# Kernel optimization log

Hardware: AMD Instinct MI355X
Metric: run time of the kernel (lower is better)

The kernel has to match this reference:

```python
import jax, jax.numpy as jnp
import numpy as np
from jax import lax

B, C, N = 128, 320, 256
H = W = 16
GROUPS = 5
RATIO = 8
MASK_EPS = 1e-6   # registered buffer 'eps' in the torch module
GN_EPS = 1e-5     # torch GroupNorm default


def setup_inputs() -> dict:
    key = jax.random.key(0)
    ks = jax.random.split(key, 10)
    def rn(k, shape, scale=0.05):
        return jax.random.normal(k, shape, dtype=jnp.float32) * scale
    return {
        "x": jax.random.normal(ks[0], (B, C, N), dtype=jnp.float32),
        "low_cutoff": jnp.float32(0.2),
        "high_cutoff": jnp.float32(0.7),
        "ca_w1": rn(ks[1], (C // RATIO, C)),
        "ca_b1": jnp.zeros((C // RATIO,), jnp.float32),
        "ca_w2": rn(ks[2], (3 * C, C // RATIO)),
        "ca_b2": jnp.zeros((3 * C,), jnp.float32),
        "low_w": rn(ks[3], (C, C, 3, 3)),
        "low_b": jnp.zeros((C,), jnp.float32),
        "low_g": jnp.ones((C,), jnp.float32),
        "low_beta": jnp.zeros((C,), jnp.float32),
        "mid_w": rn(ks[4], (C, C, 3, 3)),
        "mid_b": jnp.zeros((C,), jnp.float32),
        "mid_g": jnp.ones((C,), jnp.float32),
        "mid_beta": jnp.zeros((C,), jnp.float32),
        "high_w": rn(ks[5], (C, C, 3, 3)),
        "high_b": jnp.zeros((C,), jnp.float32),
        "high_g": jnp.ones((C,), jnp.float32),
        "high_beta": jnp.zeros((C,), jnp.float32),
        "sa_w": rn(ks[6], (1, C, 1, 1)),
        "sa_b": jnp.zeros((1,), jnp.float32),
    }


def _conv3x3_gn(y, w, b, gamma, beta):
    # Conv2d(C,C,3,padding=1) -> GroupNorm(5,C)
    out = lax.conv_general_dilated(
        y, w, window_strides=(1, 1), padding='SAME',
        dimension_numbers=('NCHW', 'OIHW', 'NCHW'))
    out = out + b[None, :, None, None]
    b_, c_, h_, w_ = out.shape
    g = out.reshape(b_, GROUPS, c_ // GROUPS, h_, w_)
    mu = g.mean(axis=(2, 3, 4), keepdims=True)
    var = g.var(axis=(2, 3, 4), keepdims=True)
    g = (g - mu) * lax.rsqrt(var + GN_EPS)
    out = g.reshape(b_, c_, h_, w_)
    return out * gamma[None, :, None, None] + beta[None, :, None, None]


def reference(x, low_cutoff, high_cutoff, ca_w1, ca_b1, ca_w2, ca_b2,
              low_w, low_b, low_g, low_beta,
              mid_w, mid_b, mid_g, mid_beta,
              high_w, high_b, high_g, high_beta,
              sa_w, sa_b):
    b, c, n = x.shape
    n_pix = H * W
    # reshape_to_square (N == n_pix here, pad/slice kept for faithfulness)
    if n < n_pix:
        xp = jnp.pad(x, ((0, 0), (0, 0), (0, n_pix - n)))
    else:
        xp = x[:, :, :n_pix]
    x2d = xp.reshape(b, c, H, W)

    # DynamicFrequencyFilter: avgpool over N -> 1x1 conv1d -> relu -> 1x1 conv1d -> sigmoid
    avg = x.mean(axis=-1)                                  # [B, C]
    hcw = jax.nn.relu(avg @ ca_w1.T + ca_b1)               # [B, C//8]
    cw = jax.nn.sigmoid(hcw @ ca_w2.T + ca_b2)             # [B, 3C]
    cw = cw.reshape(b, 3, c, 1, 1)

    # FFT + shifted frequency masks. torch fftshift(dim=None) shifts all dims,
    # but the B/C shifts commute with the (B/C-broadcast) mask multiply and are
    # undone by ifftshift, so shifting only the spatial axes is equivalent.
    fft_feat = jnp.fft.fftshift(jnp.fft.fft2(x2d), axes=(-2, -1))
    yy, xx = jnp.meshgrid(jnp.linspace(-1.0, 1.0, H), jnp.linspace(-1.0, 1.0, W), indexing='ij')
    dist = jnp.sqrt(xx ** 2 + yy ** 2) / np.sqrt(2.0)
    low_mask = jax.nn.sigmoid((low_cutoff - dist) / MASK_EPS)
    mid_mask = jax.nn.sigmoid((dist - low_cutoff) / MASK_EPS) * jax.nn.sigmoid((high_cutoff - dist) / MASK_EPS)
    high_mask = jax.nn.sigmoid((dist - high_cutoff) / MASK_EPS)

    def band(mask):
        return jnp.fft.ifft2(jnp.fft.ifftshift(fft_feat * mask, axes=(-2, -1))).real

    low_feat = _conv3x3_gn(band(low_mask), low_w, low_b, low_g, low_beta) + x2d
    mid_feat = _conv3x3_gn(band(mid_mask), mid_w, mid_b, mid_g, mid_beta) + x2d
    high_feat = _conv3x3_gn(band(high_mask), high_w, high_b, high_g, high_beta) + x2d

    fused = cw[:, 0] * low_feat + cw[:, 1] * mid_feat + cw[:, 2] * high_feat

    # spatial attention: 1x1 conv C->1, sigmoid
    sw = jax.nn.sigmoid(jnp.einsum('bchw,c->bhw', fused, sa_w[0, :, 0, 0])[:, None] + sa_b[0])
    out = (fused * sw).reshape(b, c, n_pix)
    return out[:, :, :n]
```

## Files before the change

### kernel.cpp

```cpp
#include <hip/hip_runtime.h>
#include <math.h>

#define NB 128
#define NC 320
#define NG 5
#define CPG 64
#define NHID 40

typedef short bf16x8 __attribute__((ext_vector_type(8)));
typedef short s16x4  __attribute__((ext_vector_type(4)));
typedef float f32x4  __attribute__((ext_vector_type(4)));

__device__ __forceinline__ float sigf(float x){ return 1.0f/(1.0f+expf(-x)); }

__device__ __forceinline__ unsigned short f2b(float f){
  unsigned u = __float_as_uint(f);
  unsigned r = (u + 0x7fffu + ((u >> 16) & 1u)) >> 16;
  return (unsigned short)r;
}
__device__ __forceinline__ float b2f(unsigned short u){
  return __uint_as_float(((unsigned)u) << 16);
}

__device__ __forceinline__ void gll16(const void* g, void* l){
  __builtin_amdgcn_global_load_lds(
      (const __attribute__((address_space(1))) void*)g,
      (__attribute__((address_space(3))) void*)l, 16, 0, 0);
}

__global__ __launch_bounds__(256) void k_mask(const float* __restrict__ lowc,
                                              const float* __restrict__ highc,
                                              float* __restrict__ mask){
  int t = threadIdx.x;
  int a1 = t >> 4, a2 = t & 15;
  float lc = lowc[0], hc = highc[0];
  const float step = 2.0f / 15.0f;
  float cy = -1.0f + step * (float)a1;
  float cx = -1.0f + step * (float)a2;
  float dist = sqrtf(cx*cx + cy*cy) / 1.41421356237309515f;
  mask[t]       = sigf((lc - dist) * 1e6f);
  mask[256 + t] = sigf((dist - lc) * 1e6f) * sigf((hc - dist) * 1e6f);
  mask[512 + t] = sigf((dist - hc) * 1e6f);
}

__global__ __launch_bounds__(256) void k_prepWgT(const float* __restrict__ mask,
                                                 unsigned short* __restrict__ WgT){
  __shared__ float cost[16];
  __shared__ float msh[256];
  int band = blockIdx.x >> 8, p = blockIdx.x & 255;
  int q = threadIdx.x;
  if (q < 16) cost[q] = cosf((float)q * 0.392699081698724154f);
  msh[q] = mask[band*256 + q];
  __syncthreads();
  int d1 = ((p >> 4) - (q >> 4)) & 15;
  int d2 = ((p & 15) - (q & 15)) & 15;
  float s = 0.f;
  int ang0 = (8*d1 + 8*d2) & 15;
  for (int a1 = 0; a1 < 16; ++a1){
    int ang = (ang0 + a1*d1) & 15;
    #pragma unroll
    for (int a2 = 0; a2 < 16; ++a2){
      s += msh[a1*16 + a2] * cost[ang];
      ang = (ang + d2) & 15;
    }
  }
  WgT[(size_t)(band << 16) + (p << 8) + q] = f2b(s * (1.0f/256.0f));
}

__global__ __launch_bounds__(320) void k_wt2(const float* __restrict__ w0,
                                             const float* __restrict__ w1,
                                             const float* __restrict__ w2,
                                             unsigned short* __restrict__ WAb){
  int band = blockIdx.x / 360, blk = blockIdx.x % 360;
  const float* w = band == 0 ? w0 : (band == 1 ? w1 : w2);
  int co  = threadIdx.x;
  int tap = blk / 40; int rem = blk % 40; int cib = rem >> 2; int cig = rem & 3;
  unsigned short tmp[8];
  #pragma unroll
  for (int j = 0; j < 8; ++j){
    int ci = cib*32 + cig*8 + j;
    tmp[j] = f2b(w[((size_t)co * NC + ci) * 9 + tap]);
  }
  unsigned short* dst = WAb + (size_t)band*921600 + ((size_t)blk * NC + co) * 8;
  *(s16x4*)dst       = *(s16x4*)tmp;
  *(s16x4*)(dst + 4) = *(s16x4*)(tmp + 4);
}

__global__ __launch_bounds__(256) void k_zerohalo(unsigned short* __restrict__ bandT){
  unsigned short* base = bandT + (size_t)blockIdx.x * 103680;
  for (int i = threadIdx.x; i < 5440; i += 256){
    int idx = i / 80, v = i % 80;
    int r, c;
    if (idx < 18)      { r = 0;        c = idx;      }
    else if (idx < 36) { r = 17;       c = idx - 18; }
    else if (idx < 52) { r = idx - 35; c = 0;        }
    else               { r = idx - 51; c = 17;       }
    s16x4 z = {0,0,0,0};
    *(s16x4*)(base + (size_t)(r*18 + c)*NC + v*4) = z;
  }
}

__global__ __launch_bounds__(256) void k_ca(const float* __restrict__ avg,
                                            const float* __restrict__ w1,
                                            const float* __restrict__ b1,
                                            const float* __restrict__ w2,
                                            const float* __restrict__ b2,
                                            float* __restrict__ cw){
  __shared__ float a[NC];
  __shared__ float h[NHID];
  int b = blockIdx.x, t = threadIdx.x;
  a[t] = avg[b * NC + t];
  if (t < NC - 256) a[256 + t] = avg[b * NC + 256 + t];
  __syncthreads();
  if (t < NHID){
    float s = b1[t];
    for (int i = 0; i < NC; ++i) s += w1[t * NC + i] * a[i];
    h[t] = fmaxf(s, 0.0f);
  }
  __syncthreads();
  for (int o = t; o < 3 * NC; o += 256){
    float s = b2[o];
    for (int i = 0; i < NHID; ++i) s += w2[o * NHID + i] * h[i];
    cw[b * (3 * NC) + o] = sigf(s);
  }
}

__global__ __launch_bounds__(256, 4) void k_bandg3(const float* __restrict__ x,
                                                   const unsigned short* __restrict__ WgT,
                                                   unsigned short* __restrict__ bandT,
                                                   float* __restrict__ avgOut){
  __shared__ unsigned short xt[64*256];
  int tid = threadIdx.x;
  int wgid = (blockIdx.x & 7)*80 + (blockIdx.x >> 3);
  int b = wgid / 5, cq = wgid % 5;
  int cibase = cq * 64;
  size_t rowbase = (size_t)wgid * 64;

  {
    int r = tid >> 2, c0 = (tid & 3) * 64;
    const float* xp = x + (rowbase + r)*256 + c0;
    unsigned short* dp = xt + r*256;
    int sw = (r & 7) << 3;
    float rs = 0.f;
    #pragma unroll
    for (int j = 0; j < 64; j += 4){
      float4 f = *(const float4*)(xp + j);
      rs += f.x + f.y + f.z + f.w;
      unsigned short t4[4] = { f2b(f.x), f2b(f.y), f2b(f.z), f2b(f.w) };
      *(s16x4*)(dp + ((c0 + j) ^ sw)) = *(s16x4*)t4;
    }
    rs += __shfl_down(rs, 1);
    rs += __shfl_down(rs, 2);
    if ((tid & 3) == 0) avgOut[rowbase + r] = rs * (1.0f/256.0f);
  }
  __syncthreads();

  int l  = tid & 63;
  int wq = tid >> 6;
  int cig = l >> 4, lan = l & 15;

  for (int band = 0; band < 3; ++band){
    const unsigned short* Wg = WgT + (size_t)band * 65536;
    unsigned short* bT = bandT + (size_t)band * 13271040;

    f32x4 acc[4][4];
    #pragma unroll
    for (int m = 0; m < 4; ++m)
      #pragma unroll
      for (int n = 0; n < 4; ++n) acc[m][n] = (f32x4){0.f,0.f,0.f,0.f};

    #pragma unroll 2
    for (int ks = 0; ks < 8; ++ks){
      int koff = ks*32 + cig*8;
      bf16x8 a[4], bv[4];
      #pragma unroll
      for (int m = 0; m < 4; ++m){
        int row = m*16 + lan;
        a[m] = *(const bf16x8*)(xt + row*256 + (koff ^ ((row & 7) << 3)));
      }
      #pragma unroll
      for (int n = 0; n < 4; ++n){
        int p = wq*64 + n*16 + lan;
        bv[n] = *(const bf16x8*)(Wg + (size_t)p*256 + koff);
      }
      #pragma unroll
      for (int m = 0; m < 4; ++m)
        #pragma unroll
        for (int n = 0; n < 4; ++n)
          acc[m][n] = __builtin_amdgcn_mfma_f32_16x16x32_bf16(a[m], bv[n], acc[m][n], 0, 0, 0);
    }

    #pragma unroll
    for (int m = 0; m < 4; ++m){
      #pragma unroll
      for (int n = 0; n < 4; ++n){
        int p = wq*64 + n*16 + lan;
        int slot = ((p >> 4) + 1) * 18 + (p & 15) + 1;
        int ci = cibase + m*16 + cig*4;
        unsigned short o[4] = { f2b(acc[m][n][0]), f2b(acc[m][n][1]),
                                f2b(acc[m][n][2]), f2b(acc[m][n][3]) };
        *(s16x4*)(bT + ((size_t)(b*324 + slot))*NC + ci) = *(s16x4*)o;
      }
    }
  }
}

__global__ __launch_bounds__(256, 3) void k_convg(const unsigned short* __restrict__ bandT,
                                                  const unsigned short* __restrict__ WAb,
                                                  const float* __restrict__ bias0,
                                                  const float* __restrict__ bias1,
                                                  const float* __restrict__ bias2,
                                                  unsigned short* __restrict__ convb,
                                                  float* __restrict__ stats_part){
  __shared__ char ldsA[2*10240];
  __shared__ char ldsB[2*11520];
  __shared__ float stw[4][5][2];

  int tid = threadIdx.x;
  int wgid = (blockIdx.x & 7)*192 + (blockIdx.x >> 3);
  int band = wgid / 512; int rem = wgid & 511;
  int b = rem >> 2, ch = (rem >> 1) & 1, ph = rem & 1;

  const unsigned short* bT = bandT + (size_t)band*13271040 + (size_t)b*103680;
  const unsigned short* WA = WAb + (size_t)band*921600;
  const float* bias = band == 0 ? bias0 : (band == 1 ? bias1 : bias2);
  unsigned short* cb = convb + (size_t)band * 10485760;

  int l = tid & 63, w = tid >> 6;
  int wco = w >> 1, wpx = w & 1;
  int cig = l >> 4, lan = l & 15;
  int cobase = ch*160 + wco*80;
  int px0 = ph*128 + wpx*64;

  int ga0 = tid, ga1 = tid + 256, ga2 = tid + 512;
  int aoff0 = (ga0/160)*2560 + (ga0%160)*8 + ch*1280;
  int aoff1 = (ga1/160)*2560 + (ga1%160)*8 + ch*1280;
  int aoff2 = (ga2/160)*2560 + (ga2%160)*8 + ch*1280;
  int gb0 = tid, gb1 = tid + 256, gb2 = tid + 512;
  int boff0 = (ph*144 + gb0%180)*320 + (gb0/180)*8;
  int boff1 = (ph*144 + gb1%180)*320 + (gb1/180)*8;
  int boff2 = (ph*144 + gb2%180)*320 + (gb2/180)*8;

  int Aread0 = (cig*160 + wco*80 + lan)*16;
  int Bread0 = (cig*180 + (wpx*4 + 1)*18 + lan + 1)*16;

  f32x4 acc[5][4];
  #pragma unroll
  for (int m = 0; m < 5; ++m)
    #pragma unroll
    for (int n = 0; n < 4; ++n) acc[m][n] = (f32x4){0.f,0.f,0.f,0.f};

#define STAGE_A(KN) do { \
    int tap_ = (KN)%9, cib_ = (KN)/9; \
    const unsigned short* sA = WA + (size_t)(tap_*40 + cib_*4)*2560; \
    char* dA = ldsA + ((KN)&1)*10240; \
    gll16(sA + aoff0, dA + tid*16); \
    gll16(sA + aoff1, dA + 4096 + tid*16); \
    if (tid < 128) gll16(sA + aoff2, dA + 8192 + tid*16); \
  } while(0)

#define STAGE_B(CN) do { \
    const unsigned short* sB = bT + (CN)*32; \
    char* dB = ldsB + ((CN)&1)*11520; \
    gll16(sB + boff0, dB + tid*16); \
    gll16(sB + boff1, dB + 4096 + tid*16); \
    if (tid < 208) gll16(sB + boff2, dB + 8192 + tid*16); \
  } while(0)

  STAGE_A(0);
  STAGE_B(0);
  __syncthreads();

  for (int kk = 0; kk < 90; ++kk){
    int cib = kk / 9;
    int tap = kk - cib*9;

    if (kk < 89) STAGE_A(kk + 1);
    if (tap == 0 && cib < 9) STAGE_B(cib + 1);

    int dhdw = ((tap/3)*18 + (tap - (tap/3)*3) - 19)*16;

    const char* Ab = ldsA + (kk&1)*10240 + Aread0;
    bf16x8 a0 = *(const bf16x8*)(Ab);
    bf16x8 a1 = *(const bf16x8*)(Ab + 256);
    bf16x8 a2 = *(const bf16x8*)(Ab + 512);
    bf16x8 a3 = *(const bf16x8*)(Ab + 768);
    bf16x8 a4 = *(const bf16x8*)(Ab + 1024);
    const char* Bb = ldsB + (cib&1)*11520 + Bread0 + dhdw;
    bf16x8 b0 = *(const bf16x8*)(Bb);
    bf16x8 b1 = *(const bf16x8*)(Bb + 288);
    bf16x8 b2 = *(const bf16x8*)(Bb + 576);
    bf16x8 b3 = *(const bf16x8*)(Bb + 864);

    __builtin_amdgcn_s_setprio(1);
    acc[0][0] = __builtin_amdgcn_mfma_f32_16x16x32_bf16(a0, b0, acc[0][0],0,0,0);
    acc[0][1] = __builtin_amdgcn_mfma_f32_16x16x32_bf16(a0, b1, acc[0][1],0,0,0);
    acc[0][2] = __builtin_amdgcn_mfma_f32_16x16x32_bf16(a0, b2, acc[0][2],0,0,0);
    acc[0][3] = __builtin_amdgcn_mfma_f32_16x16x32_bf16(a0, b3, acc[0][3],0,0,0);
    acc[1][0] = __builtin_amdgcn_mfma_f32_16x16x32_bf16(a1, b0, acc[1][0],0,0,0);
    acc[1][1] = __builtin_amdgcn_mfma_f32_16x16x32_bf16(a1, b1, acc[1][1],0,0,0);
    acc[1][2] = __builtin_amdgcn_mfma_f32_16x16x32_bf16(a1, b2, acc[1][2],0,0,0);
    acc[1][3] = __builtin_amdgcn_mfma_f32_16x16x32_bf16(a1, b3, acc[1][3],0,0,0);
    acc[2][0] = __builtin_amdgcn_mfma_f32_16x16x32_bf16(a2, b0, acc[2][0],0,0,0);
    acc[2][1] = __builtin_amdgcn_mfma_f32_16x16x32_bf16(a2, b1, acc[2][1],0,0,0);
    acc[2][2] = __builtin_amdgcn_mfma_f32_16x16x32_bf16(a2, b2, acc[2][2],0,0,0);
    acc[2][3] = __builtin_amdgcn_mfma_f32_16x16x32_bf16(a2, b3, acc[2][3],0,0,0);
    acc[3][0] = __builtin_amdgcn_mfma_f32_16x16x32_bf16(a3, b0, acc[3][0],0,0,0);
    acc[3][1] = __builtin_amdgcn_mfma_f32_16x16x32_bf16(a3, b1, acc[3][1],0,0,0);
    acc[3][2] = __builtin_amdgcn_mfma_f32_16x16x32_bf16(a3, b2, acc[3][2],0,0,0);
    acc[3][3] = __builtin_amdgcn_mfma_f32_16x16x32_bf16(a3, b3, acc[3][3],0,0,0);
    acc[4][0] = __builtin_amdgcn_mfma_f32_16x16x32_bf16(a4, b0, acc[4][0],0,0,0);
    acc[4][1] = __builtin_amdgcn_mfma_f32_16x16x32_bf16(a4, b1, acc[4][1],0,0,0);
    acc[4][2] = __builtin_amdgcn_mfma_f32_16x16x32_bf16(a4, b2, acc[4][2],0,0,0);
    acc[4][3] = __builtin_amdgcn_mfma_f32_16x16x32_bf16(a4, b3, acc[4][3],0,0,0);
    __builtin_amdgcn_s_setprio(0);

    __syncthreads();
  }
#undef STAGE_A
#undef STAGE_B

  #pragma unroll
  for (int m = 0; m < 5; ++m)
    #pragma unroll
    for (int r = 0; r < 4; ++r){
      float bvs = bias[cobase + m*16 + cig*4 + r];
      #pragma unroll
      for (int n = 0; n < 4; ++n) acc[m][n][r] += bvs;
    }

  #pragma unroll
  for (int m = 0; m < 5; ++m){
    float s = 0.f, q = 0.f;
    #pragma unroll
    for (int n = 0; n < 4; ++n)
      #pragma unroll
      for (int r = 0; r < 4; ++r){ float v = acc[m][n][r]; s += v; q += v*v; }
    #pragma unroll
    for (int o = 32; o > 0; o >>= 1){ s += __shfl_xor(s, o); q += __shfl_xor(q, o); }
    if (l == 0){ stw[w][m][0] = s; stw[w][m][1] = q; }
  }

  #pragma unroll
  for (int m = 0; m < 5; ++m)
    #pragma unroll
    for (int r = 0; r < 4; ++r){
      int co = cobase + m*16 + cig*4 + r;
      unsigned short* op = cb + ((size_t)(b*NC + co))*256 + px0 + lan;
      #pragma unroll
      for (int n = 0; n < 4; ++n) op[n*16] = f2b(acc[m][n][r]);
    }

  __syncthreads();
  if (tid < 6){
    int gl = tid >> 1, comp = tid & 1;
    int g = ch*2 + gl;
    float t = 0.f;
    for (int w2 = 0; w2 < 4; ++w2)
      #pragma unroll
      for (int m = 0; m < 5; ++m)
        if (((ch*160 + (w2 >> 1)*80 + m*16) >> 6) == g) t += stw[w2][m][comp];
    stats_part[((size_t)(band*NB + b)*NG + g)*8 + ch*4 + ph*2 + comp] = t;
  }
}

__global__ __launch_bounds__(512) void k_fuse3(const unsigned short* __restrict__ cb0,
                                               const unsigned short* __restrict__ cb1,
                                               const unsigned short* __restrict__ cb2,
                                               const float* __restrict__ x,
                                               const float* __restrict__ stats_part,
                                               const float* __restrict__ g0, const float* __restrict__ be0,
                                               const float* __restrict__ g1, const float* __restrict__ be1,
                                               const float* __restrict__ g2, const float* __restrict__ be2,
                                               const float* __restrict__ cw,
                                               const float* __restrict__ saw,
                                               const float* __restrict__ sab,
                                               float* __restrict__ out){
  __shared__ unsigned short fl[NC*128];
  __shared__ float mu_s[3][NG], rs_s[3][NG], sh[4][128];
  int b = blockIdx.x >> 1, half = blockIdx.x & 1;
  int tid = threadIdx.x;
  if (tid < 15){
    int band = tid / 5, g = tid % 5;
    const float* sp = stats_part + ((size_t)(band*NB + b)*NG + g)*8;
    float s = 0.f, q = 0.f;
    if (g <= 2){ s += sp[0] + sp[2]; q += sp[1] + sp[3]; }
    if (g >= 2){ s += sp[4] + sp[6]; q += sp[5] + sp[7]; }
    float mu = s * (1.f/16384.f);
    float var = q * (1.f/16384.f) - mu*mu;
    mu_s[band][g] = mu; rs_s[band][g] = rsqrtf(var + 1e-5f);
  }
  __syncthreads();

  int p = tid & 127, cs = tid >> 7;
  int px = half*128 + p;
  float sacc = 0.f;
  const float* cwb = cw + b*960;
  for (int ci = cs; ci < NC; ci += 4){
    int g = ci >> 6;
    size_t idx = ((size_t)(b*NC + ci))*256 + px;
    float xv = x[idx];
    float f =
      cwb[ci      ] * ((b2f(cb0[idx]) - mu_s[0][g])*rs_s[0][g]*g0[ci] + be0[ci] + xv) +
      cwb[320 + ci] * ((b2f(cb1[idx]) - mu_s[1][g])*rs_s[1][g]*g1[ci] + be1[ci] + xv) +
      cwb[640 + ci] * ((b2f(cb2[idx]) - mu_s[2][g])*rs_s[2][g]*g2[ci] + be2[ci] + xv);
    fl[ci*128 + p] = f2b(f);
    sacc += f * saw[ci];
  }
  sh[cs][p] = sacc;
  __syncthreads();
  if (tid < 128) sh[0][tid] = sigf(sh[0][tid] + sh[1][tid] + sh[2][tid] + sh[3][tid] + sab[0]);
  __syncthreads();
  float swv = sh[0][p];
  for (int ci = cs; ci < NC; ci += 4){
    size_t idx = ((size_t)(b*NC + ci))*256 + px;
    out[idx] = b2f(fl[ci*128 + p]) * swv;
  }
}

extern "C" void kernel_launch(void* const* d_in, const int* in_sizes, int n_in,
                              void* d_out, int out_size, void* d_ws, size_t ws_size,
                              hipStream_t stream){
  (void)in_sizes; (void)n_in; (void)out_size; (void)ws_size;
  const float* x     = (const float*)d_in[0];
  const float* lowc  = (const float*)d_in[1];
  const float* highc = (const float*)d_in[2];
  const float* ca_w1 = (const float*)d_in[3];
  const float* ca_b1 = (const float*)d_in[4];
  const float* ca_w2 = (const float*)d_in[5];
  const float* ca_b2 = (const float*)d_in[6];
  const float* conv_w[3] = {(const float*)d_in[7],  (const float*)d_in[11], (const float*)d_in[15]};
  const float* conv_b[3] = {(const float*)d_in[8],  (const float*)d_in[12], (const float*)d_in[16]};
  const float* gn_g[3]   = {(const float*)d_in[9],  (const float*)d_in[13], (const float*)d_in[17]};
  const float* gn_be[3]  = {(const float*)d_in[10], (const float*)d_in[14], (const float*)d_in[18]};
  const float* sa_w = (const float*)d_in[19];
  const float* sa_b = (const float*)d_in[20];
  float* out = (float*)d_out;

  char* base = (char*)d_ws;
  float*          mask  = (float*)base;
  unsigned short* WgT   = (unsigned short*)(base + 4096);
  unsigned short* WAb   = (unsigned short*)(base + 397312);
  unsigned short* bandT = (unsigned short*)(base + 5926912);
  unsigned short* cbb   = (unsigned short*)(base + 85553152);
  float*          cw    = (float*)(base + 148467712);
  float*          avg   = (float*)(base + 148959232);
  float*          stats = (float*)(base + 149123072);
  unsigned short* cb0 = cbb;
  unsigned short* cb1 = cbb + 10485760;
  unsigned short* cb2 = cbb + 20971520;

  k_mask    <<<1,    256, 0, stream>>>(lowc, highc, mask);
  k_prepWgT <<<768,  256, 0, stream>>>(mask, WgT);
  k_wt2     <<<1080, 320, 0, stream>>>(conv_w[0], conv_w[1], conv_w[2], WAb);
  k_zerohalo<<<384,  256, 0, stream>>>(bandT);

  k_bandg3<<<640, 256, 0, stream>>>(x, WgT, bandT, avg);
  k_ca    <<<NB,  256, 0, stream>>>(avg, ca_w1, ca_b1, ca_w2, ca_b2, cw);

  k_convg<<<1536, 256, 0, stream>>>(bandT, WAb, conv_b[0], conv_b[1], conv_b[2],
                                    cbb, stats);

  k_fuse3<<<256, 512, 0, stream>>>(cb0, cb1, cb2, x, stats,
                                   gn_g[0], gn_be[0], gn_g[1], gn_be[1], gn_g[2], gn_be[2],
                                   cw, sa_w, sa_b, out);
}
```

Before: 291.8 us.

## Triple-buffer conv weight staging with vmcnt waits; compute circulant kernel once

```diff
diff --git a/kernel.cpp b/kernel.cpp
--- a/kernel.cpp
+++ b/kernel.cpp
@@ -28,32 +28,27 @@
       (__attribute__((address_space(3))) void*)l, 16, 0, 0);
 }
 
-__global__ __launch_bounds__(256) void k_mask(const float* __restrict__ lowc,
+__global__ __launch_bounds__(256) void k_kern(const float* __restrict__ lowc,
                                               const float* __restrict__ highc,
-                                              float* __restrict__ mask){
-  int t = threadIdx.x;
-  int a1 = t >> 4, a2 = t & 15;
+                                              float* __restrict__ kern){
+  __shared__ float msh[256];
+  __shared__ float cost[16];
+  int band = blockIdx.x, t = threadIdx.x;
   float lc = lowc[0], hc = highc[0];
-  const float step = 2.0f / 15.0f;
-  float cy = -1.0f + step * (float)a1;
-  float cx = -1.0f + step * (float)a2;
-  float dist = sqrtf(cx*cx + cy*cy) / 1.41421356237309515f;
-  mask[t]       = sigf((lc - dist) * 1e6f);
-  mask[256 + t] = sigf((dist - lc) * 1e6f) * sigf((hc - dist) * 1e6f);
-  mask[512 + t] = sigf((dist - hc) * 1e6f);
-}
-
-__global__ __launch_bounds__(256) void k_prepWgT(const float* __restrict__ mask,
-                                                 unsigned short* __restrict__ WgT){
-  __shared__ float cost[16];
-  __shared__ float msh[256];
-  int band = blockIdx.x >> 8, p = blockIdx.x & 255;
-  int q = threadIdx.x;
-  if (q < 16) cost[q] = cosf((float)q * 0.392699081698724154f);
-  msh[q] = mask[band*256 + q];
-  __syncthreads();
-  int d1 = ((p >> 4) - (q >> 4)) & 15;
-  int d2 = ((p & 15) - (q & 15)) & 15;
+  {
+    int a1 = t >> 4, a2 = t & 15;
+    const float step = 2.0f / 15.0f;
+    float cy = -1.0f + step * (float)a1;
+    float cx = -1.0f + step * (float)a2;
+    float dist = sqrtf(cx*cx + cy*cy) / 1.41421356237309515f;
+    float m = band == 0 ? sigf((lc - dist) * 1e6f)
+            : band == 1 ? sigf((dist - lc) * 1e6f) * sigf((hc - dist) * 1e6f)
+                        : sigf((dist - hc) * 1e6f);
+    msh[t] = m;
+  }
+  if (t < 16) cost[t] = cosf((float)t * 0.392699081698724154f);
+  __syncthreads();
+  int d1 = t >> 4, d2 = t & 15;
   float s = 0.f;
   int ang0 = (8*d1 + 8*d2) & 15;
   for (int a1 = 0; a1 < 16; ++a1){
@@ -64,26 +59,40 @@
       ang = (ang + d2) & 15;
     }
   }
-  WgT[(size_t)(band << 16) + (p << 8) + q] = f2b(s * (1.0f/256.0f));
-}
-
-__global__ __launch_bounds__(320) void k_wt2(const float* __restrict__ w0,
+  kern[band*256 + t] = s * (1.0f/256.0f);
+}
+
+__global__ __launch_bounds__(256) void k_gather(const float* __restrict__ kern,
+                                                unsigned short* __restrict__ WgT){
+  __shared__ float ksh[256];
+  int band = blockIdx.x >> 8, p = blockIdx.x & 255, q = threadIdx.x;
+  ksh[q] = kern[band*256 + q];
+  __syncthreads();
+  int d1 = ((p >> 4) - (q >> 4)) & 15;
+  int d2 = ((p & 15) - (q & 15)) & 15;
+  WgT[(size_t)(band << 16) + (p << 8) + q] = f2b(ksh[(d1 << 4) | d2]);
+}
+
+__global__ __launch_bounds__(256) void k_wt2(const float* __restrict__ w0,
                                              const float* __restrict__ w1,
                                              const float* __restrict__ w2,
                                              unsigned short* __restrict__ WAb){
-  int band = blockIdx.x / 360, blk = blockIdx.x % 360;
+  __shared__ float wsh[2880];
+  int band = blockIdx.x / 320, co = blockIdx.x % 320;
   const float* w = band == 0 ? w0 : (band == 1 ? w1 : w2);
-  int co  = threadIdx.x;
-  int tap = blk / 40; int rem = blk % 40; int cib = rem >> 2; int cig = rem & 3;
-  unsigned short tmp[8];
-  #pragma unroll
-  for (int j = 0; j < 8; ++j){
-    int ci = cib*32 + cig*8 + j;
-    tmp[j] = f2b(w[((size_t)co * NC + ci) * 9 + tap]);
-  }
-  unsigned short* dst = WAb + (size_t)band*921600 + ((size_t)blk * NC + co) * 8;
-  *(s16x4*)dst       = *(s16x4*)tmp;
-  *(s16x4*)(dst + 4) = *(s16x4*)(tmp + 4);
+  const float* src = w + (size_t)co * 2880;
+  for (int i = threadIdx.x; i < 2880; i += 256) wsh[i] = src[i];
+  __syncthreads();
+  unsigned short* dst = WAb + (size_t)band * 921600;
+  for (int g = threadIdx.x; g < 360; g += 256){
+    int tap = g / 40, r = g % 40;
+    unsigned short tmp[8];
+    #pragma unroll
+    for (int j = 0; j < 8; ++j) tmp[j] = f2b(wsh[(r*8 + j)*9 + tap]);
+    s16x4* o = (s16x4*)(dst + (size_t)g * 2560 + co*8);
+    o[0] = *(s16x4*)tmp;
+    o[1] = *(s16x4*)(tmp + 4);
+  }
 }
 
 __global__ __launch_bounds__(256) void k_zerohalo(unsigned short* __restrict__ bandT){
@@ -212,7 +221,7 @@
                                                   const float* __restrict__ bias2,
                                                   unsigned short* __restrict__ convb,
                                                   float* __restrict__ stats_part){
-  __shared__ char ldsA[2*10240];
+  __shared__ char ldsA[3*10240];
   __shared__ char ldsB[2*11520];
   __shared__ float stw[4][5][2];
 
@@ -224,7 +233,7 @@
   const unsigned short* bT = bandT + (size_t)band*13271040 + (size_t)b*103680;
   const unsigned short* WA = WAb + (size_t)band*921600;
   const float* bias = band == 0 ? bias0 : (band == 1 ? bias1 : bias2);
-  unsigned short* cb = convb + (size_t)band * 10485760;
+  unsigned short* cbp = convb + (size_t)band * 10485760;
 
   int l = tid & 63, w = tid >> 6;
   int wco = w >> 1, wpx = w & 1;
@@ -250,10 +259,9 @@
     #pragma unroll
     for (int n = 0; n < 4; ++n) acc[m][n] = (f32x4){0.f,0.f,0.f,0.f};
 
-#define STAGE_A(KN) do { \
-    int tap_ = (KN)%9, cib_ = (KN)/9; \
-    const unsigned short* sA = WA + (size_t)(tap_*40 + cib_*4)*2560; \
-    char* dA = ldsA + ((KN)&1)*10240; \
+#define STAGE_A(TAP, CIB, BUF) do { \
+    const unsigned short* sA = WA + (size_t)((TAP)*40 + (CIB)*4)*2560; \
+    char* dA = ldsA + (BUF)*10240; \
     gll16(sA + aoff0, dA + tid*16); \
     gll16(sA + aoff1, dA + 4096 + tid*16); \
     if (tid < 128) gll16(sA + aoff2, dA + 8192 + tid*16); \
@@ -267,58 +275,75 @@
     if (tid < 208) gll16(sB + boff2, dB + 8192 + tid*16); \
   } while(0)
 
-  STAGE_A(0);
+#define VWAIT(N) asm volatile("s_waitcnt vmcnt(" #N ")" ::: "memory")
+
+  STAGE_A(0, 0, 0);
   STAGE_B(0);
-  __syncthreads();
-
-  for (int kk = 0; kk < 90; ++kk){
-    int cib = kk / 9;
-    int tap = kk - cib*9;
-
-    if (kk < 89) STAGE_A(kk + 1);
-    if (tap == 0 && cib < 9) STAGE_B(cib + 1);
-
-    int dhdw = ((tap/3)*18 + (tap - (tap/3)*3) - 19)*16;
-
-    const char* Ab = ldsA + (kk&1)*10240 + Aread0;
-    bf16x8 a0 = *(const bf16x8*)(Ab);
-    bf16x8 a1 = *(const bf16x8*)(Ab + 256);
-    bf16x8 a2 = *(const bf16x8*)(Ab + 512);
-    bf16x8 a3 = *(const bf16x8*)(Ab + 768);
-    bf16x8 a4 = *(const bf16x8*)(Ab + 1024);
-    const char* Bb = ldsB + (cib&1)*11520 + Bread0 + dhdw;
-    bf16x8 b0 = *(const bf16x8*)(Bb);
-    bf16x8 b1 = *(const bf16x8*)(Bb + 288);
-    bf16x8 b2 = *(const bf16x8*)(Bb + 576);
-    bf16x8 b3 = *(const bf16x8*)(Bb + 864);
-
-    __builtin_amdgcn_s_setprio(1);
-    acc[0][0] = __builtin_amdgcn_mfma_f32_16x16x32_bf16(a0, b0, acc[0][0],0,0,0);
-    acc[0][1] = __builtin_amdgcn_mfma_f32_16x16x32_bf16(a0, b1, acc[0][1],0,0,0);
-    acc[0][2] = __builtin_amdgcn_mfma_f32_16x16x32_bf16(a0, b2, acc[0][2],0,0,0);
-    acc[0][3] = __builtin_amdgcn_mfma_f32_16x16x32_bf16(a0, b3, acc[0][3],0,0,0);
-    acc[1][0] = __builtin_amdgcn_mfma_f32_16x16x32_bf16(a1, b0, acc[1][0],0,0,0);
-    acc[1][1] = __builtin_amdgcn_mfma_f32_16x16x32_bf16(a1, b1, acc[1][1],0,0,0);
-    acc[1][2] = __builtin_amdgcn_mfma_f32_16x16x32_bf16(a1, b2, acc[1][2],0,0,0);
-    acc[1][3] = __builtin_amdgcn_mfma_f32_16x16x32_bf16(a1, b3, acc[1][3],0,0,0);
-    acc[2][0] = __builtin_amdgcn_mfma_f32_16x16x32_bf16(a2, b0, acc[2][0],0,0,0);
-    acc[2][1] = __builtin_amdgcn_mfma_f32_16x16x32_bf16(a2, b1, acc[2][1],0,0,0);
-    acc[2][2] = __builtin_amdgcn_mfma_f32_16x16x32_bf16(a2, b2, acc[2][2],0,0,0);
-    acc[2][3] = __builtin_amdgcn_mfma_f32_16x16x32_bf16(a2, b3, acc[2][3],0,0,0);
-    acc[3][0] = __builtin_amdgcn_mfma_f32_16x16x32_bf16(a3, b0, acc[3][0],0,0,0);
-    acc[3][1] = __builtin_amdgcn_mfma_f32_16x16x32_bf16(a3, b1, acc[3][1],0,0,0);
-    acc[3][2] = __builtin_amdgcn_mfma_f32_16x16x32_bf16(a3, b2, acc[3][2],0,0,0);
-    acc[3][3] = __builtin_amdgcn_mfma_f32_16x16x32_bf16(a3, b3, acc[3][3],0,0,0);
-    acc[4][0] = __builtin_amdgcn_mfma_f32_16x16x32_bf16(a4, b0, acc[4][0],0,0,0);
-    acc[4][1] = __builtin_amdgcn_mfma_f32_16x16x32_bf16(a4, b1, acc[4][1],0,0,0);
-    acc[4][2] = __builtin_amdgcn_mfma_f32_16x16x32_bf16(a4, b2, acc[4][2],0,0,0);
-    acc[4][3] = __builtin_amdgcn_mfma_f32_16x16x32_bf16(a4, b3, acc[4][3],0,0,0);
-    __builtin_amdgcn_s_setprio(0);
-
-    __syncthreads();
+  STAGE_A(1, 0, 1);
+  VWAIT(2);
+  __builtin_amdgcn_s_barrier();
+
+  for (int cib = 0; cib < 10; ++cib){
+    #pragma unroll
+    for (int tap = 0; tap < 9; ++tap){
+      const char* Ab = ldsA + (tap % 3)*10240 + Aread0;
+      bf16x8 a0 = *(const bf16x8*)(Ab);
+      bf16x8 a1 = *(const bf16x8*)(Ab + 256);
+      bf16x8 a2 = *(const bf16x8*)(Ab + 512);
+      bf16x8 a3 = *(const bf16x8*)(Ab + 768);
+      bf16x8 a4 = *(const bf16x8*)(Ab + 1024);
+      const int dhdw = ((tap/3)*18 + (tap%3) - 19)*16;
+      const char* Bb = ldsB + (cib & 1)*11520 + Bread0 + dhdw;
+      bf16x8 b0 = *(const bf16x8*)(Bb);
+      bf16x8 b1 = *(const bf16x8*)(Bb + 288);
+      bf16x8 b2 = *(const bf16x8*)(Bb + 576);
+      bf16x8 b3 = *(const bf16x8*)(Bb + 864);
+
+      if (tap <= 6){
+        STAGE_A(tap + 2, cib, (tap + 2) % 3);
+      } else if (cib < 9){
+        STAGE_A(tap - 7, cib + 1, (tap + 2) % 3);
+      }
+      if (tap == 0 && cib < 9) STAGE_B(cib + 1);
+
+      __builtin_amdgcn_s_setprio(1);
+      acc[0][0] = __builtin_amdgcn_mfma_f32_16x16x32_bf16(a0, b0, acc[0][0],0,0,0);
+      acc[0][1] = __builtin_amdgcn_mfma_f32_16x16x32_bf16(a0, b1, acc[0][1],0,0,0);
+      acc[0][2] = __builtin_amdgcn_mfma_f32_16x16x32_bf16(a0, b2, acc[0][2],0,0,0);
+      acc[0][3] = __builtin_amdgcn_mfma_f32_16x16x32_bf16(a0, b3, acc[0][3],0,0,0);
+      acc[1][0] = __builtin_amdgcn_mfma_f32_16x16x32_bf16(a1, b0, acc[1][0],0,0,0);
+      acc[1][1] = __builtin_amdgcn_mfma_f32_16x16x32_bf16(a1, b1, acc[1][1],0,0,0);
+      acc[1][2] = __builtin_amdgcn_mfma_f32_16x16x32_bf16(a1, b2, acc[1][2],0,0,0);
+      acc[1][3] = __builtin_amdgcn_mfma_f32_16x16x32_bf16(a1, b3, acc[1][3],0,0,0);
+      acc[2][0] = __builtin_amdgcn_mfma_f32_16x16x32_bf16(a2, b0, acc[2][0],0,0,0);
+      acc[2][1] = __builtin_amdgcn_mfma_f32_16x16x32_bf16(a2, b1, acc[2][1],0,0,0);
+      acc[2][2] = __builtin_amdgcn_mfma_f32_16x16x32_bf16(a2, b2, acc[2][2],0,0,0);
+      acc[2][3] = __builtin_amdgcn_mfma_f32_16x16x32_bf16(a2, b3, acc[2][3],0,0,0);
+      acc[3][0] = __builtin_amdgcn_mfma_f32_16x16x32_bf16(a3, b0, acc[3][0],0,0,0);
+      acc[3][1] = __builtin_amdgcn_mfma_f32_16x16x32_bf16(a3, b1, acc[3][1],0,0,0);
+      acc[3][2] = __builtin_amdgcn_mfma_f32_16x16x32_bf16(a3, b2, acc[3][2],0,0,0);
+      acc[3][3] = __builtin_amdgcn_mfma_f32_16x16x32_bf16(a3, b3, acc[3][3],0,0,0);
+      acc[4][0] = __builtin_amdgcn_mfma_f32_16x16x32_bf16(a4, b0, acc[4][0],0,0,0);
+      acc[4][1] = __builtin_amdgcn_mfma_f32_16x16x32_bf16(a4, b1, acc[4][1],0,0,0);
+      acc[4][2] = __builtin_amdgcn_mfma_f32_16x16x32_bf16(a4, b2, acc[4][2],0,0,0);
+      acc[4][3] = __builtin_amdgcn_mfma_f32_16x16x32_bf16(a4, b3, acc[4][3],0,0,0);
+      __builtin_amdgcn_s_setprio(0);
+
+      if (tap <= 1){
+        if (cib < 9) { VWAIT(5); } else { VWAIT(2); }
+      } else if (tap == 7){
+        if (cib < 9) { VWAIT(2); } else { VWAIT(0); }
+      } else if (tap == 8){
+        if (cib < 9) { VWAIT(2); }
+      } else {
+        VWAIT(2);
+      }
+      if (!(cib == 9 && tap == 8)) __builtin_amdgcn_s_barrier();
+    }
   }
 #undef STAGE_A
 #undef STAGE_B
+#undef VWAIT
 
   #pragma unroll
   for (int m = 0; m < 5; ++m)
@@ -346,7 +371,7 @@
     #pragma unroll
     for (int r = 0; r < 4; ++r){
       int co = cobase + m*16 + cig*4 + r;
-      unsigned short* op = cb + ((size_t)(b*NC + co))*256 + px0 + lan;
+      unsigned short* op = cbp + ((size_t)(b*NC + co))*256 + px0 + lan;
       #pragma unroll
       for (int n = 0; n < 4; ++n) op[n*16] = f2b(acc[m][n][r]);
     }
@@ -438,7 +463,7 @@
   float* out = (float*)d_out;
 
   char* base = (char*)d_ws;
-  float*          mask  = (float*)base;
+  float*          kern  = (float*)base;
   unsigned short* WgT   = (unsigned short*)(base + 4096);
   unsigned short* WAb   = (unsigned short*)(base + 397312);
   unsigned short* bandT = (unsigned short*)(base + 5926912);
@@ -450,9 +475,9 @@
   unsigned short* cb1 = cbb + 10485760;
   unsigned short* cb2 = cbb + 20971520;
 
-  k_mask    <<<1,    256, 0, stream>>>(lowc, highc, mask);
-  k_prepWgT <<<768,  256, 0, stream>>>(mask, WgT);
-  k_wt2     <<<1080, 320, 0, stream>>>(conv_w[0], conv_w[1], conv_w[2], WAb);
+  k_kern    <<<3,    256, 0, stream>>>(lowc, highc, kern);
+  k_gather  <<<768,  256, 0, stream>>>(kern, WgT);
+  k_wt2     <<<960,  256, 0, stream>>>(conv_w[0], conv_w[1], conv_w[2], WAb);
   k_zerohalo<<<384,  256, 0, stream>>>(bandT);
 
   k_bandg3<<<640, 256, 0, stream>>>(x, WgT, bandT, avg);
```

Result: faster. 280.1 us (-4.0%).
